# Kernel tuning notes

Hardware: AMD Instinct MI355X
Metric: run time of the kernel (lower is better)

The kernel has to match this reference:

```python
import jax, jax.numpy as jnp
import numpy as np

MARGIN = 0.5
EPS = 1e-8  # torch CosineSimilarity eps


def setup_inputs() -> dict:
    key = jax.random.key(0)
    k1, k2 = jax.random.split(key)
    line_end_embeddings = jax.random.normal(k1, (4096, 32, 256), dtype=jnp.float32)
    rhyme_scheme = jax.random.randint(k2, (4096, 32), 0, 4, dtype=jnp.int32)
    return {"line_end_embeddings": line_end_embeddings, "rhyme_scheme": rhyme_scheme}


def reference(line_end_embeddings, rhyme_scheme):
    b, n, d = line_end_embeddings.shape
    # cosine similarity with torch-style eps clamping on norms
    norms = jnp.maximum(jnp.linalg.norm(line_end_embeddings, axis=-1, keepdims=True), EPS)
    unit = line_end_embeddings / norms                       # [b, n, d]
    sims = jnp.einsum("bid,bjd->bij", unit, unit)            # [b, n, n]
    same = rhyme_scheme[:, :, None] == rhyme_scheme[:, None, :]  # [b, n, n]
    per_pair = jnp.where(same, 1.0 - sims, jax.nn.relu(sims - MARGIN))
    # only pairs i < j (strict upper triangle)
    upper = jnp.triu(jnp.ones((n, n), dtype=bool), k=1)
    total = jnp.sum(per_pair * upper[None, :, :])
    count = b * (n * (n - 1) // 2)
    return total / max(count, 1)
```

## Files before the change

kernel.cpp:

```cpp
#include <hip/hip_runtime.h>
#include <hip/hip_bf16.h>
#include <stdint.h>


typedef short bf16x8 __attribute__((ext_vector_type(8)));
typedef float f32x4  __attribute__((ext_vector_type(4)));

#define MARGIN 0.5f
#define EPS_NORM 1e-8f
#define NPAIR_INV (1.0f / 2031616.0f)

static __device__ __forceinline__ short f2bf(float f) {
    unsigned u = __float_as_uint(f);
    u += 0x7fffu + ((u >> 16) & 1u);
    return (short)(u >> 16);
}

__global__ __launch_bounds__(256, 8) void rhyme_loss_kernel(
    const float* __restrict__ emb,
    const int*   __restrict__ sch,
    float*       __restrict__ out)
{
    __shared__ f32x4 s_acc[3][3][64];
    __shared__ float s_diag[32];
    __shared__ float s_inv[32];
    __shared__ int   s_sch[32];

    const int t    = threadIdx.x;
    const int wv   = t >> 6;
    const int lane = t & 63;
    const int b    = blockIdx.x;

    const int q = lane >> 4;
    const int c = lane & 15;

    if (t < 32)
        s_sch[t] = sch[(size_t)b * 32 + t];

    const float* base0 = emb + (size_t)b * 8192 + (size_t)c * 256 + wv * 64 + q * 8;
    const float* base1 = base0 + 16 * 256;

    f32x4 acc00 = {0.f, 0.f, 0.f, 0.f};
    f32x4 acc01 = {0.f, 0.f, 0.f, 0.f};
    f32x4 acc11 = {0.f, 0.f, 0.f, 0.f};

    #pragma unroll
    for (int kc = 0; kc < 64; kc += 32) {
        float4 a0 = *(const float4*)(base0 + kc);
        float4 a1 = *(const float4*)(base0 + kc + 4);
        float4 b0 = *(const float4*)(base1 + kc);
        float4 b1 = *(const float4*)(base1 + kc + 4);

        bf16x8 f0, f1;
        f0[0] = f2bf(a0.x); f0[1] = f2bf(a0.y); f0[2] = f2bf(a0.z); f0[3] = f2bf(a0.w);
        f0[4] = f2bf(a1.x); f0[5] = f2bf(a1.y); f0[6] = f2bf(a1.z); f0[7] = f2bf(a1.w);
        f1[0] = f2bf(b0.x); f1[1] = f2bf(b0.y); f1[2] = f2bf(b0.z); f1[3] = f2bf(b0.w);
        f1[4] = f2bf(b1.x); f1[5] = f2bf(b1.y); f1[6] = f2bf(b1.z); f1[7] = f2bf(b1.w);

        acc00 = __builtin_amdgcn_mfma_f32_16x16x32_bf16(f0, f0, acc00, 0, 0, 0);
        acc01 = __builtin_amdgcn_mfma_f32_16x16x32_bf16(f0, f1, acc01, 0, 0, 0);
        acc11 = __builtin_amdgcn_mfma_f32_16x16x32_bf16(f1, f1, acc11, 0, 0, 0);
    }

    if (wv != 0) {
        s_acc[wv - 1][0][lane] = acc00;
        s_acc[wv - 1][1][lane] = acc01;
        s_acc[wv - 1][2][lane] = acc11;
    }
    __syncthreads();

    if (wv == 0) {
        #pragma unroll
        for (int p = 0; p < 3; ++p) {
            acc00 += s_acc[p][0][lane];
            acc01 += s_acc[p][1][lane];
            acc11 += s_acc[p][2][lane];
        }

        const int dreg = c - 4 * q;
        if (dreg >= 0 && dreg < 4) {
            s_diag[c]      = acc00[dreg];
            s_diag[16 + c] = acc11[dreg];
        }
        __builtin_amdgcn_wave_barrier();
        if (lane < 32)
            s_inv[lane] = 1.0f / fmaxf(sqrtf(s_diag[lane]), EPS_NORM);
        __builtin_amdgcn_wave_barrier();

        const float invj0 = s_inv[c];
        const float invj1 = s_inv[16 + c];
        const int   sj0   = s_sch[c];
        const int   sj1   = s_sch[16 + c];

        float sum = 0.0f;
        #pragma unroll
        for (int r = 0; r < 4; ++r) {
            const int   i0    = q * 4 + r;
            const float inv_i = s_inv[i0];
            const int   si    = s_sch[i0];

            {
                float sim = acc01[r] * inv_i * invj1;
                sum += (si == sj1) ? (1.0f - sim) : fmaxf(sim - MARGIN, 0.0f);
            }
            if (i0 < c) {
                float sim = acc00[r] * inv_i * invj0;
                sum += (si == sj0) ? (1.0f - sim) : fmaxf(sim - MARGIN, 0.0f);
                float sim2 = acc11[r] * s_inv[16 + i0] * invj1;
                sum += (s_sch[16 + i0] == sj1) ? (1.0f - sim2)
                                               : fmaxf(sim2 - MARGIN, 0.0f);
            }
        }

        #pragma unroll
        for (int off = 32; off > 0; off >>= 1)
            sum += __shfl_down(sum, off, 64);

        if (lane == 0)
            atomicAdd(out, sum * NPAIR_INV);
    }
}

extern "C" void kernel_launch(void* const* d_in, const int* in_sizes, int n_in,
                              void* d_out, int out_size, void* d_ws, size_t ws_size,
                              hipStream_t stream) {
    const float* emb = (const float*)d_in[0];
    const int*   sch = (const int*)d_in[1];
    float*       out = (float*)d_out;

    hipMemsetAsync(out, 0, sizeof(float), stream);
    rhyme_loss_kernel<<<dim3(4096), dim3(256), 0, stream>>>(emb, sch, out);
}
```

Measured before the change: 206.9 us.

## Stage coalesced bf16 tiles in LDS and process two batches per block with prefetch

Each block now handles two batch items. The whole 32x256 tile is loaded with fully coalesced float4 reads, converted to bf16 into padded shared memory, and the MFMA fragments are read from there. The next batch's tile is prefetched into registers while the current one is computed. This is meant to replace the strided per-lane global loads with coalesced traffic, overlap loading with compute, and halve the grid size. It adds extra block barriers and LDS traffic, and it drops the occupancy hint from the launch bounds.

After: 209.9 us. Within noise of the previous version (+1.4%).

```diff
diff --git a/kernel.cpp b/kernel.cpp
--- a/kernel.cpp
+++ b/kernel.cpp
@@ -4,11 +4,14 @@
 
 
 typedef short bf16x8 __attribute__((ext_vector_type(8)));
+typedef short bf16x4 __attribute__((ext_vector_type(4)));
 typedef float f32x4  __attribute__((ext_vector_type(4)));
 
 #define MARGIN 0.5f
 #define EPS_NORM 1e-8f
 #define NPAIR_INV (1.0f / 2031616.0f)
+#define ROW_S 264
+#define NBLK  2048
 
 static __device__ __forceinline__ short f2bf(float f) {
     unsigned u = __float_as_uint(f);
@@ -16,108 +19,127 @@
     return (short)(u >> 16);
 }
 
-__global__ __launch_bounds__(256, 8) void rhyme_loss_kernel(
+__global__ __launch_bounds__(256) void rhyme_loss_kernel(
     const float* __restrict__ emb,
     const int*   __restrict__ sch,
     float*       __restrict__ out)
 {
-    __shared__ f32x4 s_acc[3][3][64];
+    __shared__ f32x4 s_mem[1056];
+    short* s_stage = (short*)s_mem;
+    f32x4 (*s_acc)[3][64] = (f32x4 (*)[3][64])s_mem;
     __shared__ float s_diag[32];
     __shared__ float s_inv[32];
-    __shared__ int   s_sch[32];
+    __shared__ int   s_sch2[2][32];
 
     const int t    = threadIdx.x;
     const int wv   = t >> 6;
     const int lane = t & 63;
-    const int b    = blockIdx.x;
+    const int q    = lane >> 4;
+    const int c    = lane & 15;
 
-    const int q = lane >> 4;
-    const int c = lane & 15;
+    if (t < 64)
+        s_sch2[t >> 5][t & 31] =
+            sch[((size_t)blockIdx.x + (size_t)(t >> 5) * NBLK) * 32 + (t & 31)];
 
-    if (t < 32)
-        s_sch[t] = sch[(size_t)b * 32 + t];
+    const float* gb = emb + (size_t)blockIdx.x * 8192;
+    float4 pf[8];
+    #pragma unroll
+    for (int r = 0; r < 8; ++r)
+        pf[r] = *(const float4*)(gb + r * 1024 + 4 * t);
 
-    const float* base0 = emb + (size_t)b * 8192 + (size_t)c * 256 + wv * 64 + q * 8;
-    const float* base1 = base0 + 16 * 256;
-
-    f32x4 acc00 = {0.f, 0.f, 0.f, 0.f};
-    f32x4 acc01 = {0.f, 0.f, 0.f, 0.f};
-    f32x4 acc11 = {0.f, 0.f, 0.f, 0.f};
-
-    #pragma unroll
-    for (int kc = 0; kc < 64; kc += 32) {
-        float4 a0 = *(const float4*)(base0 + kc);
-        float4 a1 = *(const float4*)(base0 + kc + 4);
-        float4 b0 = *(const float4*)(base1 + kc);
-        float4 b1 = *(const float4*)(base1 + kc + 4);
-
-        bf16x8 f0, f1;
-        f0[0] = f2bf(a0.x); f0[1] = f2bf(a0.y); f0[2] = f2bf(a0.z); f0[3] = f2bf(a0.w);
-        f0[4] = f2bf(a1.x); f0[5] = f2bf(a1.y); f0[6] = f2bf(a1.z); f0[7] = f2bf(a1.w);
-        f1[0] = f2bf(b0.x); f1[1] = f2bf(b0.y); f1[2] = f2bf(b0.z); f1[3] = f2bf(b0.w);
-        f1[4] = f2bf(b1.x); f1[5] = f2bf(b1.y); f1[6] = f2bf(b1.z); f1[7] = f2bf(b1.w);
-
-        acc00 = __builtin_amdgcn_mfma_f32_16x16x32_bf16(f0, f0, acc00, 0, 0, 0);
-        acc01 = __builtin_amdgcn_mfma_f32_16x16x32_bf16(f0, f1, acc01, 0, 0, 0);
-        acc11 = __builtin_amdgcn_mfma_f32_16x16x32_bf16(f1, f1, acc11, 0, 0, 0);
-    }
-
-    if (wv != 0) {
-        s_acc[wv - 1][0][lane] = acc00;
-        s_acc[wv - 1][1][lane] = acc01;
-        s_acc[wv - 1][2][lane] = acc11;
-    }
-    __syncthreads();
-
-    if (wv == 0) {
+    for (int it = 0; it < 2; ++it) {
         #pragma unroll
-        for (int p = 0; p < 3; ++p) {
-            acc00 += s_acc[p][0][lane];
-            acc01 += s_acc[p][1][lane];
-            acc11 += s_acc[p][2][lane];
+        for (int r = 0; r < 8; ++r) {
+            bf16x4 h;
+            h[0] = f2bf(pf[r].x); h[1] = f2bf(pf[r].y);
+            h[2] = f2bf(pf[r].z); h[3] = f2bf(pf[r].w);
+            *(bf16x4*)(&s_stage[(4 * r + wv) * ROW_S + 4 * lane]) = h;
         }
 
-        const int dreg = c - 4 * q;
-        if (dreg >= 0 && dreg < 4) {
-            s_diag[c]      = acc00[dreg];
-            s_diag[16 + c] = acc11[dreg];
-        }
-        __builtin_amdgcn_wave_barrier();
-        if (lane < 32)
-            s_inv[lane] = 1.0f / fmaxf(sqrtf(s_diag[lane]), EPS_NORM);
-        __builtin_amdgcn_wave_barrier();
-
-        const float invj0 = s_inv[c];
-        const float invj1 = s_inv[16 + c];
-        const int   sj0   = s_sch[c];
-        const int   sj1   = s_sch[16 + c];
-
-        float sum = 0.0f;
-        #pragma unroll
-        for (int r = 0; r < 4; ++r) {
-            const int   i0    = q * 4 + r;
-            const float inv_i = s_inv[i0];
-            const int   si    = s_sch[i0];
-
-            {
-                float sim = acc01[r] * inv_i * invj1;
-                sum += (si == sj1) ? (1.0f - sim) : fmaxf(sim - MARGIN, 0.0f);
-            }
-            if (i0 < c) {
-                float sim = acc00[r] * inv_i * invj0;
-                sum += (si == sj0) ? (1.0f - sim) : fmaxf(sim - MARGIN, 0.0f);
-                float sim2 = acc11[r] * s_inv[16 + i0] * invj1;
-                sum += (s_sch[16 + i0] == sj1) ? (1.0f - sim2)
-                                               : fmaxf(sim2 - MARGIN, 0.0f);
-            }
+        if (it == 0) {
+            const float* gb1 = emb + ((size_t)blockIdx.x + NBLK) * 8192;
+            #pragma unroll
+            for (int r = 0; r < 8; ++r)
+                pf[r] = *(const float4*)(gb1 + r * 1024 + 4 * t);
         }
 
+        __syncthreads();
+
+        f32x4 a00 = {0.f, 0.f, 0.f, 0.f};
+        f32x4 a01 = {0.f, 0.f, 0.f, 0.f};
+        f32x4 a11 = {0.f, 0.f, 0.f, 0.f};
         #pragma unroll
-        for (int off = 32; off > 0; off >>= 1)
-            sum += __shfl_down(sum, off, 64);
+        for (int ch = 0; ch < 2; ++ch) {
+            const short* p0 = s_stage + c * ROW_S + wv * 64 + ch * 32 + q * 8;
+            const short* p1 = p0 + 16 * ROW_S;
+            bf16x8 f0 = *(const bf16x8*)p0;
+            bf16x8 f1 = *(const bf16x8*)p1;
+            a00 = __builtin_amdgcn_mfma_f32_16x16x32_bf16(f0, f0, a00, 0, 0, 0);
+            a01 = __builtin_amdgcn_mfma_f32_16x16x32_bf16(f0, f1, a01, 0, 0, 0);
+            a11 = __builtin_amdgcn_mfma_f32_16x16x32_bf16(f1, f1, a11, 0, 0, 0);
+        }
 
-        if (lane == 0)
-            atomicAdd(out, sum * NPAIR_INV);
+        __syncthreads();
+
+        if (wv != 0) {
+            s_acc[wv - 1][0][lane] = a00;
+            s_acc[wv - 1][1][lane] = a01;
+            s_acc[wv - 1][2][lane] = a11;
+        }
+        __syncthreads();
+
+        if (wv == 0) {
+            #pragma unroll
+            for (int p = 0; p < 3; ++p) {
+                a00 += s_acc[p][0][lane];
+                a01 += s_acc[p][1][lane];
+                a11 += s_acc[p][2][lane];
+            }
+
+            const int dreg = c - 4 * q;
+            if (dreg >= 0 && dreg < 4) {
+                s_diag[c]      = a00[dreg];
+                s_diag[16 + c] = a11[dreg];
+            }
+            __builtin_amdgcn_wave_barrier();
+            if (lane < 32)
+                s_inv[lane] = 1.0f / fmaxf(sqrtf(s_diag[lane]), EPS_NORM);
+            __builtin_amdgcn_wave_barrier();
+
+            const float invj0 = s_inv[c];
+            const float invj1 = s_inv[16 + c];
+            const int   sj0   = s_sch2[it][c];
+            const int   sj1   = s_sch2[it][16 + c];
+
+            float sum = 0.0f;
+            #pragma unroll
+            for (int r = 0; r < 4; ++r) {
+                const int   i0    = q * 4 + r;
+                const float inv_i = s_inv[i0];
+                const int   si    = s_sch2[it][i0];
+
+                {
+                    float sim = a01[r] * inv_i * invj1;
+                    sum += (si == sj1) ? (1.0f - sim) : fmaxf(sim - MARGIN, 0.0f);
+                }
+                if (i0 < c) {
+                    float sim = a00[r] * inv_i * invj0;
+                    sum += (si == sj0) ? (1.0f - sim) : fmaxf(sim - MARGIN, 0.0f);
+                    float sim2 = a11[r] * s_inv[16 + i0] * invj1;
+                    sum += (s_sch2[it][16 + i0] == sj1) ? (1.0f - sim2)
+                                                        : fmaxf(sim2 - MARGIN, 0.0f);
+                }
+            }
+
+            #pragma unroll
+            for (int off = 32; off > 0; off >>= 1)
+                sum += __shfl_down(sum, off, 64);
+
+            if (lane == 0)
+                atomicAdd(out, sum * NPAIR_INV);
+        }
+
+        __syncthreads();
     }
 }
 
@@ -129,5 +151,5 @@
     float*       out = (float*)d_out;
 
     hipMemsetAsync(out, 0, sizeof(float), stream);
-    rhyme_loss_kernel<<<dim3(4096), dim3(256), 0, stream>>>(emb, sch, out);
+    rhyme_loss_kernel<<<dim3(NBLK), dim3(256), 0, stream>>>(emb, sch, out);
 }
```
